# Kernel tuning notes

Measured on AMD Instinct MI355X. Metric: run time of the kernel, lower is better.

Reference implementation:

```python
import jax, jax.numpy as jnp
import numpy as np

N_NODES = 100000
N_EDGES = 1000000
D_NODE = 64
D_EDGE = 32
D_OUT = 64
EPS = 1e-07
BETA = 1.0


def setup_inputs() -> dict:
    key = jax.random.key(0)
    ks = jax.random.split(key, 6)
    node_feats = jax.random.normal(ks[0], (N_NODES, D_NODE), dtype=jnp.float32)
    edge_feats = jax.random.normal(ks[1], (N_EDGES, D_EDGE), dtype=jnp.float32)
    src = jax.random.randint(ks[2], (N_EDGES,), 0, N_NODES, dtype=jnp.int32)
    dst = jax.random.randint(ks[3], (N_EDGES,), 0, N_NODES, dtype=jnp.int32)
    We = jax.random.normal(ks[4], (D_EDGE, D_OUT), dtype=jnp.float32) / np.sqrt(D_EDGE)
    be = jnp.zeros((D_OUT,), dtype=jnp.float32)
    Wm = jax.random.normal(ks[5], (D_NODE, D_OUT), dtype=jnp.float32) / np.sqrt(D_NODE)
    bm = jnp.zeros((D_OUT,), dtype=jnp.float32)
    return {"node_feats": node_feats, "edge_feats": edge_feats, "src": src,
            "dst": dst, "We": We, "be": be, "Wm": Wm, "bm": bm}


def reference(node_feats, edge_feats, src, dst, We, be, Wm, bm):
    n = node_feats.shape[0]
    # edge encoder + u_add_e: m_e = h_src + Linear(e)
    m = node_feats[src] + (edge_feats @ We + be)          # [E, D]
    m = jax.nn.relu(m) + EPS
    # segmented (per-destination) softmax over edges, per feature channel
    z = m * BETA
    zmax = jax.ops.segment_max(z, dst, num_segments=n)    # [N, D]
    ez = jnp.exp(z - zmax[dst])                           # [E, D]
    denom = jax.ops.segment_sum(ez, dst, num_segments=n)  # [N, D]
    a = ez / denom[dst]                                   # [E, D]
    # weighted scatter-sum aggregation
    agg = jax.ops.segment_sum(m * a, dst, num_segments=n) # [N, D]
    feats = node_feats + agg
    # mlp_layers=1 -> single Linear
    return feats @ Wm + bm
```

## Files before the change

kernel.cpp:

```cpp
#include <hip/hip_runtime.h>

#define D_NODE 64
#define D_EDGE 32
#define D_OUT  64
#define EPSF   1e-7f
#define CAP    48
#define CHUNK  16

typedef const __attribute__((address_space(1))) unsigned int guint_t;
typedef __attribute__((address_space(3))) unsigned int luint_t;

__global__ __launch_bounds__(256) void genconv_build_kernel(
    const int* __restrict__ src,
    const int* __restrict__ dst,
    int* __restrict__ cnt,
    int2* __restrict__ slots,
    int E)
{
    const int e = blockIdx.x * blockDim.x + threadIdx.x;
    if (e >= E) return;
    const int d = dst[e];
    const int pos = atomicAdd(&cnt[d], 1);
    if (pos < CAP)
        slots[d * CAP + pos] = make_int2(e, src[e]);
}

__global__ __launch_bounds__(256, 6) void genconv_gather_kernel(
    const float* __restrict__ node,
    const float* __restrict__ ef,
    const int*  __restrict__ cnt,
    const int2* __restrict__ slots,
    const float* __restrict__ We,
    const float* __restrict__ be,
    const float* __restrict__ Wm,
    const float* __restrict__ bm,
    float* __restrict__ out,
    int N)
{
    __shared__ float wm_s[D_NODE * D_OUT];
    __shared__ __align__(16) float efs[4][CHUNK * D_EDGE];
    __shared__ __align__(16) float fbuf[4][D_NODE];

    for (int i = threadIdx.x; i < D_NODE * D_OUT; i += blockDim.x)
        wm_s[i] = Wm[i];
    __syncthreads();

    const int lane  = (int)(threadIdx.x & 63);
    const int wslot = (int)(threadIdx.x >> 6);
    float* const efw = efs[wslot];

    float w[D_EDGE];
#pragma unroll
    for (int k = 0; k < D_EDGE; ++k)
        w[k] = We[k * D_OUT + lane];
    const float bias_e = be[lane];
    const float bias_m = bm[lane];

    const int wid = (int)((blockIdx.x * blockDim.x + threadIdx.x) >> 6);
    const int nw  = (int)((gridDim.x * blockDim.x) >> 6);

    int n = wid;
    int   c_pf   = 0;
    int2  sl_pf  = make_int2(0, 0);
    float res_pf = 0.0f;
    if (n < N) {
        c_pf   = cnt[n];
        sl_pf  = (lane < CAP) ? slots[n * CAP + lane] : make_int2(0, 0);
        res_pf = node[(size_t)n * D_NODE + lane];
    }

    while (n < N) {
        const int c = min(c_pf, CAP);
        const int e_l = (lane < c) ? sl_pf.x : 0;
        const int s_l = (lane < c) ? sl_pf.y : 0;
        const float fres = res_pf;

        const int n_next = n + nw;
        if (n_next < N) {
            c_pf   = cnt[n_next];
            sl_pf  = (lane < CAP) ? slots[n_next * CAP + lane] : make_int2(0, 0);
            res_pf = node[(size_t)n_next * D_NODE + lane];
        }

        float num = 0.0f, den = 0.0f;

        for (int base = 0; base < c; base += CHUNK) {
            const int cc = min(CHUNK, c - base);

            {
                const int r0 = base + (lane >> 3);
                const int er0 = __builtin_amdgcn_ds_bpermute(r0 << 2, e_l);
                const float* g0 = ef + (size_t)er0 * D_EDGE + ((lane & 7) << 2);
                __builtin_amdgcn_global_load_lds((guint_t*)g0, (luint_t*)&efw[0], 16, 0, 0);
                const int er1 = __builtin_amdgcn_ds_bpermute((r0 + 8) << 2, e_l);
                const float* g1 = ef + (size_t)er1 * D_EDGE + ((lane & 7) << 2);
                __builtin_amdgcn_global_load_lds((guint_t*)g1, (luint_t*)&efw[8 * D_EDGE], 16, 0, 0);
            }

            float h0a[CHUNK / 2], h1a[CHUNK / 2];
#pragma unroll
            for (int p = 0; p < CHUNK / 2; ++p) {
                if (2 * p < cc) {
                    const int i0 = base + 2 * p;
                    const int i1 = (2 * p + 1 < cc) ? i0 + 1 : i0;
                    const int s0 = __builtin_amdgcn_readlane(s_l, i0);
                    const int s1 = __builtin_amdgcn_readlane(s_l, i1);
                    h0a[p] = node[(size_t)s0 * D_NODE + lane];
                    h1a[p] = node[(size_t)s1 * D_NODE + lane];
                }
            }

            asm volatile("s_waitcnt vmcnt(0)" ::: "memory");
            __builtin_amdgcn_sched_barrier(0);

#pragma unroll
            for (int p = 0; p < CHUNK / 2; ++p) {
                if (2 * p < cc) {
                    const float* eb0 = efw + (2 * p) * D_EDGE;
                    const float* eb1 = efw + (2 * p + 1) * D_EDGE;
                    float v0 = bias_e, v1 = bias_e;
                    float v0b = 0.0f, v1b = 0.0f;
#pragma unroll
                    for (int k4 = 0; k4 < 4; ++k4) {
                        const float4 a0 = *(const float4*)(eb0 + k4 * 4);
                        const float4 b0 = *(const float4*)(eb0 + 16 + k4 * 4);
                        const float4 a1 = *(const float4*)(eb1 + k4 * 4);
                        const float4 b1 = *(const float4*)(eb1 + 16 + k4 * 4);
                        v0  = fmaf(a0.x, w[4 * k4 + 0], v0);
                        v0  = fmaf(a0.y, w[4 * k4 + 1], v0);
                        v0  = fmaf(a0.z, w[4 * k4 + 2], v0);
                        v0  = fmaf(a0.w, w[4 * k4 + 3], v0);
                        v0b = fmaf(b0.x, w[16 + 4 * k4 + 0], v0b);
                        v0b = fmaf(b0.y, w[16 + 4 * k4 + 1], v0b);
                        v0b = fmaf(b0.z, w[16 + 4 * k4 + 2], v0b);
                        v0b = fmaf(b0.w, w[16 + 4 * k4 + 3], v0b);
                        v1  = fmaf(a1.x, w[4 * k4 + 0], v1);
                        v1  = fmaf(a1.y, w[4 * k4 + 1], v1);
                        v1  = fmaf(a1.z, w[4 * k4 + 2], v1);
                        v1  = fmaf(a1.w, w[4 * k4 + 3], v1);
                        v1b = fmaf(b1.x, w[16 + 4 * k4 + 0], v1b);
                        v1b = fmaf(b1.y, w[16 + 4 * k4 + 1], v1b);
                        v1b = fmaf(b1.z, w[16 + 4 * k4 + 2], v1b);
                        v1b = fmaf(b1.w, w[16 + 4 * k4 + 3], v1b);
                    }
                    const float m0 = fmaxf(h0a[p] + v0 + v0b, 0.0f) + EPSF;
                    const float z0 = __expf(m0);
                    num = fmaf(m0, z0, num);
                    den += z0;
                    if (2 * p + 1 < cc) {
                        const float m1 = fmaxf(h1a[p] + v1 + v1b, 0.0f) + EPSF;
                        const float z1 = __expf(m1);
                        num = fmaf(m1, z1, num);
                        den += z1;
                    }
                }
            }
            __builtin_amdgcn_sched_barrier(0);
        }

        float f = fres;
        if (c > 0)
            f += num / den;

        fbuf[wslot][lane] = f;
        float acc = bias_m;
#pragma unroll
        for (int d4 = 0; d4 < D_NODE / 4; ++d4) {
            const float4 fv = *(const float4*)&fbuf[wslot][d4 * 4];
            acc = fmaf(fv.x, wm_s[(d4 * 4 + 0) * D_OUT + lane], acc);
            acc = fmaf(fv.y, wm_s[(d4 * 4 + 1) * D_OUT + lane], acc);
            acc = fmaf(fv.z, wm_s[(d4 * 4 + 2) * D_OUT + lane], acc);
            acc = fmaf(fv.w, wm_s[(d4 * 4 + 3) * D_OUT + lane], acc);
        }
        out[(size_t)n * D_NODE + lane] = acc;

        n = n_next;
    }
}

extern "C" void kernel_launch(void* const* d_in, const int* in_sizes, int n_in,
                              void* d_out, int out_size, void* d_ws, size_t ws_size,
                              hipStream_t stream)
{
    const float* node = (const float*)d_in[0];
    const float* ef   = (const float*)d_in[1];
    const int*   src  = (const int*)d_in[2];
    const int*   dst  = (const int*)d_in[3];
    const float* We   = (const float*)d_in[4];
    const float* be   = (const float*)d_in[5];
    const float* Wm   = (const float*)d_in[6];
    const float* bm   = (const float*)d_in[7];
    float* out = (float*)d_out;

    const int N = in_sizes[0] / D_NODE;
    const int E = in_sizes[2];

    int*  cnt   = (int*)d_ws;
    int2* slots = (int2*)(cnt + N);

    hipMemsetAsync(cnt, 0, (size_t)N * sizeof(int), stream);

    genconv_build_kernel<<<(E + 255) / 256, 256, 0, stream>>>(src, dst, cnt, slots, E);

    genconv_gather_kernel<<<1536, 256, 0, stream>>>(node, ef, cnt, slots,
                                                    We, be, Wm, bm, out, N);
}
```

Measured before the change: 452.5 us.

## Double-buffer edge-feature and source-node gathers across 8-edge chunks

```diff
diff --git a/kernel.cpp b/kernel.cpp
--- a/kernel.cpp
+++ b/kernel.cpp
@@ -5,7 +5,7 @@
 #define D_OUT  64
 #define EPSF   1e-7f
 #define CAP    48
-#define CHUNK  16
+#define CHUNK  8
 
 typedef const __attribute__((address_space(1))) unsigned int guint_t;
 typedef __attribute__((address_space(3))) unsigned int luint_t;
@@ -25,7 +25,7 @@
         slots[d * CAP + pos] = make_int2(e, src[e]);
 }
 
-__global__ __launch_bounds__(256, 6) void genconv_gather_kernel(
+__global__ __launch_bounds__(256) void genconv_gather_kernel(
     const float* __restrict__ node,
     const float* __restrict__ ef,
     const int*  __restrict__ cnt,
@@ -38,7 +38,7 @@
     int N)
 {
     __shared__ float wm_s[D_NODE * D_OUT];
-    __shared__ __align__(16) float efs[4][CHUNK * D_EDGE];
+    __shared__ __align__(16) float efs[4][2][CHUNK * D_EDGE];
     __shared__ __align__(16) float fbuf[4][D_NODE];
 
     for (int i = threadIdx.x; i < D_NODE * D_OUT; i += blockDim.x)
@@ -47,7 +47,8 @@
 
     const int lane  = (int)(threadIdx.x & 63);
     const int wslot = (int)(threadIdx.x >> 6);
-    float* const efw = efs[wslot];
+    float* const efA = efs[wslot][0];
+    float* const efB = efs[wslot][1];
 
     float w[D_EDGE];
 #pragma unroll
@@ -69,6 +70,8 @@
         res_pf = node[(size_t)n * D_NODE + lane];
     }
 
+    struct HB { float h0, h1, h2, h3, h4, h5, h6, h7; };
+
     while (n < N) {
         const int c = min(c_pf, CAP);
         const int e_l = (lane < c) ? sl_pf.x : 0;
@@ -81,81 +84,93 @@
             sl_pf  = (lane < CAP) ? slots[n_next * CAP + lane] : make_int2(0, 0);
             res_pf = node[(size_t)n_next * D_NODE + lane];
         }
+        __builtin_amdgcn_sched_barrier(0);
 
         float num = 0.0f, den = 0.0f;
 
-        for (int base = 0; base < c; base += CHUNK) {
-            const int cc = min(CHUNK, c - base);
-
-            {
-                const int r0 = base + (lane >> 3);
-                const int er0 = __builtin_amdgcn_ds_bpermute(r0 << 2, e_l);
-                const float* g0 = ef + (size_t)er0 * D_EDGE + ((lane & 7) << 2);
-                __builtin_amdgcn_global_load_lds((guint_t*)g0, (luint_t*)&efw[0], 16, 0, 0);
-                const int er1 = __builtin_amdgcn_ds_bpermute((r0 + 8) << 2, e_l);
-                const float* g1 = ef + (size_t)er1 * D_EDGE + ((lane & 7) << 2);
-                __builtin_amdgcn_global_load_lds((guint_t*)g1, (luint_t*)&efw[8 * D_EDGE], 16, 0, 0);
+        auto stage = [&](int base, float* dstLDS) {
+            const int r  = base + (lane >> 3);
+            const int er = __builtin_amdgcn_ds_bpermute(r << 2, e_l);
+            const float* g = ef + (size_t)er * D_EDGE + ((lane & 7) << 2);
+            __builtin_amdgcn_global_load_lds((guint_t*)g, (luint_t*)dstLDS, 16, 0, 0);
+        };
+        auto hload = [&](int base, HB& H) {
+            const int s0 = __builtin_amdgcn_readlane(s_l, base + 0);
+            const int s1 = __builtin_amdgcn_readlane(s_l, base + 1);
+            const int s2 = __builtin_amdgcn_readlane(s_l, base + 2);
+            const int s3 = __builtin_amdgcn_readlane(s_l, base + 3);
+            const int s4 = __builtin_amdgcn_readlane(s_l, base + 4);
+            const int s5 = __builtin_amdgcn_readlane(s_l, base + 5);
+            const int s6 = __builtin_amdgcn_readlane(s_l, base + 6);
+            const int s7 = __builtin_amdgcn_readlane(s_l, base + 7);
+            H.h0 = node[(size_t)s0 * D_NODE + lane];
+            H.h1 = node[(size_t)s1 * D_NODE + lane];
+            H.h2 = node[(size_t)s2 * D_NODE + lane];
+            H.h3 = node[(size_t)s3 * D_NODE + lane];
+            H.h4 = node[(size_t)s4 * D_NODE + lane];
+            H.h5 = node[(size_t)s5 * D_NODE + lane];
+            H.h6 = node[(size_t)s6 * D_NODE + lane];
+            H.h7 = node[(size_t)s7 * D_NODE + lane];
+        };
+        auto pairop = [&](float ha, float hb, const float* eb0, bool second_ok) {
+            const float* eb1 = eb0 + D_EDGE;
+            float v0 = bias_e, v1 = bias_e;
+#pragma unroll
+            for (int k4 = 0; k4 < 8; ++k4) {
+                const float4 a0 = *(const float4*)(eb0 + k4 * 4);
+                const float4 a1 = *(const float4*)(eb1 + k4 * 4);
+                v0 = fmaf(a0.x, w[4 * k4 + 0], v0);
+                v0 = fmaf(a0.y, w[4 * k4 + 1], v0);
+                v0 = fmaf(a0.z, w[4 * k4 + 2], v0);
+                v0 = fmaf(a0.w, w[4 * k4 + 3], v0);
+                v1 = fmaf(a1.x, w[4 * k4 + 0], v1);
+                v1 = fmaf(a1.y, w[4 * k4 + 1], v1);
+                v1 = fmaf(a1.z, w[4 * k4 + 2], v1);
+                v1 = fmaf(a1.w, w[4 * k4 + 3], v1);
             }
-
-            float h0a[CHUNK / 2], h1a[CHUNK / 2];
-#pragma unroll
-            for (int p = 0; p < CHUNK / 2; ++p) {
-                if (2 * p < cc) {
-                    const int i0 = base + 2 * p;
-                    const int i1 = (2 * p + 1 < cc) ? i0 + 1 : i0;
-                    const int s0 = __builtin_amdgcn_readlane(s_l, i0);
-                    const int s1 = __builtin_amdgcn_readlane(s_l, i1);
-                    h0a[p] = node[(size_t)s0 * D_NODE + lane];
-                    h1a[p] = node[(size_t)s1 * D_NODE + lane];
+            const float m0 = fmaxf(ha + v0, 0.0f) + EPSF;
+            const float z0 = __expf(m0);
+            num = fmaf(m0, z0, num);
+            den += z0;
+            if (second_ok) {
+                const float m1 = fmaxf(hb + v1, 0.0f) + EPSF;
+                const float z1 = __expf(m1);
+                num = fmaf(m1, z1, num);
+                den += z1;
+            }
+        };
+        auto consume = [&](const float* eb, HB& H, int base) {
+            if (base + 0 < c) pairop(H.h0, H.h1, eb + 0 * D_EDGE, base + 1 < c);
+            if (base + 2 < c) pairop(H.h2, H.h3, eb + 2 * D_EDGE, base + 3 < c);
+            if (base + 4 < c) pairop(H.h4, H.h5, eb + 4 * D_EDGE, base + 5 < c);
+            if (base + 6 < c) pairop(H.h6, H.h7, eb + 6 * D_EDGE, base + 7 < c);
+        };
+
+        const int nch = (c + CHUNK - 1) >> 3;
+        if (nch > 0) {
+            HB HA, HB_;
+            stage(0, efA);
+            hload(0, HA);
+            for (int p = 0; ; ) {
+                {
+                    const bool more = (p + 1 < nch);
+                    if (more) { stage((p + 1) * CHUNK, efB); hload((p + 1) * CHUNK, HB_); }
+                    if (more) asm volatile("s_waitcnt vmcnt(9)" ::: "memory");
+                    else      asm volatile("s_waitcnt vmcnt(0)" ::: "memory");
+                    __builtin_amdgcn_sched_barrier(0);
+                    consume(efA, HA, p * CHUNK);
+                    if (++p >= nch) break;
+                }
+                {
+                    const bool more = (p + 1 < nch);
+                    if (more) { stage((p + 1) * CHUNK, efA); hload((p + 1) * CHUNK, HA); }
+                    if (more) asm volatile("s_waitcnt vmcnt(9)" ::: "memory");
+                    else      asm volatile("s_waitcnt vmcnt(0)" ::: "memory");
+                    __builtin_amdgcn_sched_barrier(0);
+                    consume(efB, HB_, p * CHUNK);
+                    if (++p >= nch) break;
                 }
             }
-
-            asm volatile("s_waitcnt vmcnt(0)" ::: "memory");
-            __builtin_amdgcn_sched_barrier(0);
-
-#pragma unroll
-            for (int p = 0; p < CHUNK / 2; ++p) {
-                if (2 * p < cc) {
-                    const float* eb0 = efw + (2 * p) * D_EDGE;
-                    const float* eb1 = efw + (2 * p + 1) * D_EDGE;
-                    float v0 = bias_e, v1 = bias_e;
-                    float v0b = 0.0f, v1b = 0.0f;
-#pragma unroll
-                    for (int k4 = 0; k4 < 4; ++k4) {
-                        const float4 a0 = *(const float4*)(eb0 + k4 * 4);
-                        const float4 b0 = *(const float4*)(eb0 + 16 + k4 * 4);
-                        const float4 a1 = *(const float4*)(eb1 + k4 * 4);
-                        const float4 b1 = *(const float4*)(eb1 + 16 + k4 * 4);
-                        v0  = fmaf(a0.x, w[4 * k4 + 0], v0);
-                        v0  = fmaf(a0.y, w[4 * k4 + 1], v0);
-                        v0  = fmaf(a0.z, w[4 * k4 + 2], v0);
-                        v0  = fmaf(a0.w, w[4 * k4 + 3], v0);
-                        v0b = fmaf(b0.x, w[16 + 4 * k4 + 0], v0b);
-                        v0b = fmaf(b0.y, w[16 + 4 * k4 + 1], v0b);
-                        v0b = fmaf(b0.z, w[16 + 4 * k4 + 2], v0b);
-                        v0b = fmaf(b0.w, w[16 + 4 * k4 + 3], v0b);
-                        v1  = fmaf(a1.x, w[4 * k4 + 0], v1);
-                        v1  = fmaf(a1.y, w[4 * k4 + 1], v1);
-                        v1  = fmaf(a1.z, w[4 * k4 + 2], v1);
-                        v1  = fmaf(a1.w, w[4 * k4 + 3], v1);
-                        v1b = fmaf(b1.x, w[16 + 4 * k4 + 0], v1b);
-                        v1b = fmaf(b1.y, w[16 + 4 * k4 + 1], v1b);
-                        v1b = fmaf(b1.z, w[16 + 4 * k4 + 2], v1b);
-                        v1b = fmaf(b1.w, w[16 + 4 * k4 + 3], v1b);
-                    }
-                    const float m0 = fmaxf(h0a[p] + v0 + v0b, 0.0f) + EPSF;
-                    const float z0 = __expf(m0);
-                    num = fmaf(m0, z0, num);
-                    den += z0;
-                    if (2 * p + 1 < cc) {
-                        const float m1 = fmaxf(h1a[p] + v1 + v1b, 0.0f) + EPSF;
-                        const float z1 = __expf(m1);
-                        num = fmaf(m1, z1, num);
-                        den += z1;
-                    }
-                }
-            }
-            __builtin_amdgcn_sched_barrier(0);
         }
 
         float f = fres;
@@ -202,6 +217,6 @@
 
     genconv_build_kernel<<<(E + 255) / 256, 256, 0, stream>>>(src, dst, cnt, slots, E);
 
-    genconv_gather_kernel<<<1536, 256, 0, stream>>>(node, ef, cnt, slots,
+    genconv_gather_kernel<<<2048, 256, 0, stream>>>(node, ef, cnt, slots,
                                                     We, be, Wm, bm, out, N);
 }
```

Result: faster. 379.2 us (-16.2%).
